# Kernel optimization log

Hardware: AMD Instinct MI355X
Metric: run time of the kernel (lower is better)

## Reference

```python
import jax, jax.numpy as jnp
import numpy as np

D_MODEL = 1024
N_HEADS = 16
D_HEAD = D_MODEL // N_HEADS


def setup_inputs() -> dict:
    key = jax.random.key(0)
    ks = jax.random.split(key, 5)
    scale = 1.0 / np.sqrt(D_MODEL)
    return {
        "x": jax.random.normal(ks[0], (2, 2048, D_MODEL), dtype=jnp.float32),
        "W_q": jax.random.normal(ks[1], (D_MODEL, D_MODEL), dtype=jnp.float32) * scale,
        "W_k": jax.random.normal(ks[2], (D_MODEL, D_MODEL), dtype=jnp.float32) * scale,
        "W_v": jax.random.normal(ks[3], (D_MODEL, D_MODEL), dtype=jnp.float32) * scale,
        "W_o": jax.random.normal(ks[4], (D_MODEL, D_MODEL), dtype=jnp.float32) * scale,
    }


def reference(x, W_q, W_k, W_v, W_o):
    B, S, _ = x.shape
    # nn.Linear computes x @ W.T; weights stored [out, in]
    def proj(W):
        y = jnp.einsum("bsd,ed->bse", x, W)
        return y.reshape(B, S, N_HEADS, D_HEAD).transpose(0, 2, 1, 3)  # [B,H,S,Dh]

    q, k, v = proj(W_q), proj(W_k), proj(W_v)
    scores = jnp.einsum("bhqd,bhkd->bhqk", q, k) / jnp.sqrt(jnp.float32(D_HEAD))
    causal = jnp.triu(jnp.ones((S, S), dtype=bool), k=1)
    scores = jnp.where(causal, -jnp.inf, scores)
    attn = jax.nn.softmax(scores, axis=-1)
    out = jnp.einsum("bhqk,bhkd->bhqd", attn, v)  # [B,H,S,Dh]
    out = out.transpose(0, 2, 1, 3).reshape(B, S, D_MODEL)
    return jnp.einsum("bsd,ed->bse", out, W_o)
```

## Files before the change

kernel.cpp:

```cpp
#include <hip/hip_runtime.h>


#define DMODEL 1024
#define NHEADS 16
#define DHEAD  64
#define SEQ    2048
#define BATCH  2
#define MROWS  (BATCH * SEQ)

typedef __bf16 bf16x8 __attribute__((ext_vector_type(8)));
typedef __bf16 bf16x4 __attribute__((ext_vector_type(4)));
typedef float  f32x4  __attribute__((ext_vector_type(4)));

__device__ __forceinline__ f32x4 mfma16(bf16x8 a, bf16x8 b, f32x4 c) {
    return __builtin_amdgcn_mfma_f32_16x16x32_bf16(a, b, c, 0, 0, 0);
}

__device__ __forceinline__ float max3f(float a, float b, float c) {
    return fmaxf(fmaxf(a, b), c);
}

__device__ __forceinline__ bf16x8 ld8(const float* p) {
    const f32x4 a0 = *(const f32x4*)p;
    const f32x4 a1 = *(const f32x4*)(p + 4);
    bf16x8 v;
    v[0] = (__bf16)a0[0]; v[1] = (__bf16)a0[1];
    v[2] = (__bf16)a0[2]; v[3] = (__bf16)a0[3];
    v[4] = (__bf16)a1[0]; v[5] = (__bf16)a1[1];
    v[6] = (__bf16)a1[2]; v[7] = (__bf16)a1[3];
    return v;
}

__device__ __forceinline__ void gll16(const __bf16* g, __bf16* l) {
    __builtin_amdgcn_global_load_lds(
        (const __attribute__((address_space(1))) void*)g,
        (__attribute__((address_space(3))) void*)l,
        16, 0, 0);
}

__global__ __launch_bounds__(256) void cvt_kernel(const float* __restrict__ x,
                                                  const float* __restrict__ Wq,
                                                  const float* __restrict__ Wk,
                                                  const float* __restrict__ Wv,
                                                  const float* __restrict__ Wo,
                                                  __bf16* __restrict__ xb,
                                                  __bf16* __restrict__ wcat) {
    const int y = blockIdx.y;
    const float* src;
    __bf16* dst;
    int nchunks;
    if (y == 0) { src = x; dst = xb; nchunks = (MROWS * DMODEL) / 8; }
    else {
        src = (y == 1) ? Wq : (y == 2) ? Wk : (y == 3) ? Wv : Wo;
        dst = wcat + (size_t)(y - 1) * DMODEL * DMODEL;
        nchunks = (DMODEL * DMODEL) / 8;
    }
    const int c = blockIdx.x * 256 + threadIdx.x;
    if (c < nchunks) *(bf16x8*)(dst + (size_t)c * 8) = ld8(src + (size_t)c * 8);
}

template <typename TC>
__device__ __forceinline__ void gemm_bb_body(const __bf16* __restrict__ A,
                                             const __bf16* __restrict__ W,
                                             TC* __restrict__ C,
                                             __bf16* __restrict__ VT,
                                             bool vt, int m0, int bn0, int cn0,
                                             float scale) {
    constexpr int K = DMODEL;
    __shared__ __align__(16) __bf16 As[128][32];
    __shared__ __align__(16) __bf16 Bs[128][32];

    const int tid  = threadIdx.x;
    const int lane = tid & 63;
    const int wave = tid >> 6;
    const int quad = lane >> 4;
    const int l16  = lane & 15;
    const int wm   = wave & 1;
    const int wn   = wave >> 1;

    const int srow = lane >> 2;
    const int scol = (lane & 3) * 8;

    const __bf16* a0p = A + (size_t)(m0 + wave * 16 + srow) * K + scol;
    const __bf16* a1p = A + (size_t)(m0 + 64 + wave * 16 + srow) * K + scol;
    const __bf16* b0p = W + (size_t)(bn0 + wave * 16 + srow) * K + scol;
    const __bf16* b1p = W + (size_t)(bn0 + 64 + wave * 16 + srow) * K + scol;

    f32x4 acc[4][4] = {};

    for (int k0 = 0; k0 < K; k0 += 32) {
        __syncthreads();
        gll16(a0p + k0, &As[wave * 16][0]);
        gll16(a1p + k0, &As[64 + wave * 16][0]);
        gll16(b0p + k0, &Bs[wave * 16][0]);
        gll16(b1p + k0, &Bs[64 + wave * 16][0]);
        __syncthreads();

        bf16x8 af[4], bfr[4];
#pragma unroll
        for (int i = 0; i < 4; ++i) {
            af[i]  = *(const bf16x8*)(&As[wm * 64 + i * 16 + l16][quad * 8]);
            bfr[i] = *(const bf16x8*)(&Bs[wn * 64 + i * 16 + l16][quad * 8]);
        }
#pragma unroll
        for (int mi = 0; mi < 4; ++mi)
#pragma unroll
            for (int ni = 0; ni < 4; ++ni)
                acc[mi][ni] = mfma16(af[mi], bfr[ni], acc[mi][ni]);
    }

    if (!vt) {
#pragma unroll
        for (int mi = 0; mi < 4; ++mi)
#pragma unroll
            for (int ni = 0; ni < 4; ++ni)
#pragma unroll
                for (int r = 0; r < 4; ++r) {
                    int row = m0 + wm * 64 + mi * 16 + quad * 4 + r;
                    int col = cn0 + wn * 64 + ni * 16 + l16;
                    C[(size_t)row * DMODEL + col] = (TC)(acc[mi][ni][r] * scale);
                }
    } else {
#pragma unroll
        for (int mi = 0; mi < 4; ++mi)
#pragma unroll
            for (int ni = 0; ni < 4; ++ni) {
                const int m  = m0 + wm * 64 + mi * 16 + quad * 4;
                const int hd = cn0 + wn * 64 + ni * 16 + l16;
                bf16x4 v4;
#pragma unroll
                for (int r = 0; r < 4; ++r) v4[r] = (__bf16)acc[mi][ni][r];
                *(bf16x4*)(VT + (size_t)hd * MROWS + m) = v4;
            }
    }
}

#define QSCALE 0.1803368801111204f

__global__ __launch_bounds__(256) void qkv_kernel(const __bf16* __restrict__ X,
                                                  const __bf16* __restrict__ wcat,
                                                  __bf16* __restrict__ Q,
                                                  __bf16* __restrict__ K,
                                                  __bf16* __restrict__ VT) {
    const int bn0 = blockIdx.x * 128;
    const int z   = bn0 >> 10;
    const int cn0 = bn0 - (z << 10);
    __bf16* Y = (z == 0) ? Q : K;
    const float scale = (z == 0) ? QSCALE : 1.0f;
    gemm_bb_body<__bf16>(X, wcat, Y, VT, z == 2,
                         blockIdx.y * 128, bn0, cn0, scale);
}

__global__ __launch_bounds__(256) void out_gemm_kernel(const __bf16* __restrict__ A,
                                                       const __bf16* __restrict__ W,
                                                       float* __restrict__ C) {
    gemm_bb_body<float>(A, W, C, nullptr, false,
                        blockIdx.y * 128, blockIdx.x * 128, blockIdx.x * 128, 1.0f);
}

__global__ __launch_bounds__(256) void attn_kernel(const __bf16* __restrict__ Q,
                                                   const __bf16* __restrict__ Kg,
                                                   const __bf16* __restrict__ VTg,
                                                   __bf16* __restrict__ O) {
    const int bh  = blockIdx.x;
    const int y   = blockIdx.y;
    const int ya  = y >> 3, yr = y & 7;
    const int qt2 = (ya == 0) ? (31 - yr)
                  : (ya == 1) ? (16 + yr)
                  : (ya == 2) ? (15 - yr)
                  :             yr;
    const int b = bh >> 4, h = bh & 15;
    const size_t base = (size_t)b * SEQ * DMODEL + (size_t)h * DHEAD;

    const int tid  = threadIdx.x;
    const int lane = tid & 63;
    const int wave = tid >> 6;
    const int quad = lane >> 4;
    const int l16  = lane & 15;

    __shared__ __align__(16) __bf16 Ks[64][64];
    __shared__ __align__(16) __bf16 Vs[64][64];
    __shared__ __align__(16) __bf16 Ps[4][2][16][40];

    const int sr = lane >> 3;
    const int sc = ((lane & 7) ^ sr) * 8;

    const int qrow = qt2 * 64 + wave * 16 + l16;

    const bf16x8 qf0 = *(const bf16x8*)(Q + base + (size_t)qrow * DMODEL + quad * 8);
    const bf16x8 qf1 = *(const bf16x8*)(Q + base + (size_t)qrow * DMODEL + 32 + quad * 8);

    const __bf16* kp = Kg + base + (size_t)(wave * 16 + sr) * DMODEL + sc;
    const __bf16* vp = VTg + (size_t)(h * 64 + wave * 16 + sr) * MROWS
                           + (size_t)b * SEQ + sc;

    bf16x8 ones;
#pragma unroll
    for (int i = 0; i < 8; ++i) ones[i] = (__bf16)1.0f;

    f32x4 oacc[4] = {};
    f32x4 lacc = {};
    float m_i = -1e30f;

    const int ntiles = qt2 + 1;
    const int gsw = (l16 & 7);

    for (int kt = 0; kt < ntiles; ++kt) {
        const int k0 = kt * 64;
        __syncthreads();
        {
            const __bf16* kpt = kp + (size_t)k0 * DMODEL;
            const __bf16* vpt = vp + k0;
            gll16(kpt, &Ks[wave * 16][0]);
            gll16(kpt + (size_t)8 * DMODEL, &Ks[wave * 16 + 8][0]);
            gll16(vpt, &Vs[wave * 16][0]);
            gll16(vpt + (size_t)8 * MROWS, &Vs[wave * 16 + 8][0]);
        }
        __syncthreads();

        const bool diag = (kt == ntiles - 1);

        f32x4 s[4];
#pragma unroll
        for (int g = 0; g < 4; ++g) {
            const bf16x8 kfa = *(const bf16x8*)(&Ks[g * 16 + l16][(quad ^ gsw) * 8]);
            const bf16x8 kfb = *(const bf16x8*)(&Ks[g * 16 + l16][((quad + 4) ^ gsw) * 8]);
            f32x4 t = {};
            t = mfma16(kfa, qf0, t);
            t = mfma16(kfb, qf1, t);
            s[g] = t;
        }

        float mx;
        bool ok[4][4];
        if (!diag) {
            const float t0 = max3f(s[0][0], s[0][1], s[0][2]);
            const float t1 = max3f(s[0][3], s[1][0], s[1][1]);
            const float t2 = max3f(s[1][2], s[1][3], s[2][0]);
            const float t3 = max3f(s[2][1], s[2][2], s[2][3]);
            const float t4 = max3f(s[3][0], s[3][1], s[3][2]);
            mx = max3f(max3f(t0, t1, t2), fmaxf(t3, t4), s[3][3]);
        } else {
            float v[4][4];
#pragma unroll
            for (int g = 0; g < 4; ++g)
#pragma unroll
                for (int r = 0; r < 4; ++r) {
                    const int kk = k0 + g * 16 + quad * 4 + r;
                    ok[g][r] = (kk <= qrow);
                    v[g][r] = ok[g][r] ? s[g][r] : -1e30f;
                }
            const float t0 = max3f(v[0][0], v[0][1], v[0][2]);
            const float t1 = max3f(v[0][3], v[1][0], v[1][1]);
            const float t2 = max3f(v[1][2], v[1][3], v[2][0]);
            const float t3 = max3f(v[2][1], v[2][2], v[2][3]);
            const float t4 = max3f(v[3][0], v[3][1], v[3][2]);
            mx = max3f(max3f(t0, t1, t2), fmaxf(t3, t4), v[3][3]);
        }
        mx = fmaxf(mx, __shfl_xor(mx, 16));
        mx = fmaxf(mx, __shfl_xor(mx, 32));

        const bool defer = __all(mx - m_i <= 8.0f);
        float mnew;
        if (defer) {
            mnew = m_i;
        } else {
            mnew = fmaxf(m_i, mx);
            const float alpha = exp2f(m_i - mnew);
            m_i = mnew;
#pragma unroll
            for (int f = 0; f < 4; ++f) oacc[f] *= alpha;
            lacc *= alpha;
        }

        bf16x4 w4[4];
        if (!diag) {
#pragma unroll
            for (int g = 0; g < 4; ++g)
#pragma unroll
                for (int r = 0; r < 4; ++r)
                    w4[g][r] = (__bf16)exp2f(s[g][r] - mnew);
        } else {
#pragma unroll
            for (int g = 0; g < 4; ++g)
#pragma unroll
                for (int r = 0; r < 4; ++r)
                    w4[g][r] = (__bf16)(ok[g][r] ? exp2f(s[g][r] - mnew) : 0.f);
        }

#pragma unroll
        for (int g = 0; g < 4; ++g)
            *(bf16x4*)(&Ps[wave][g >> 1][l16][(g & 1) * 16 + quad * 4]) = w4[g];

        const bf16x8 pf0 = *(const bf16x8*)(&Ps[wave][0][l16][quad * 8]);
        const bf16x8 pf1 = *(const bf16x8*)(&Ps[wave][1][l16][quad * 8]);
        lacc = mfma16(ones, pf0, lacc);
        lacc = mfma16(ones, pf1, lacc);
#pragma unroll
        for (int f = 0; f < 4; ++f) {
            const bf16x8 vfa = *(const bf16x8*)(&Vs[f * 16 + l16][(quad ^ gsw) * 8]);
            const bf16x8 vfb = *(const bf16x8*)(&Vs[f * 16 + l16][((quad + 4) ^ gsw) * 8]);
            f32x4 t = oacc[f];
            t = mfma16(vfa, pf0, t);
            t = mfma16(vfb, pf1, t);
            oacc[f] = t;
        }
    }

    const float l_i = lacc[0];
    const float inv = (l_i > 0.f) ? (1.f / l_i) : 0.f;
#pragma unroll
    for (int f = 0; f < 4; ++f) {
        bf16x4 o;
#pragma unroll
        for (int r = 0; r < 4; ++r) o[r] = (__bf16)(oacc[f][r] * inv);
        *(bf16x4*)(O + base + (size_t)qrow * DMODEL + f * 16 + quad * 4) = o;
    }
}

extern "C" void kernel_launch(void* const* d_in, const int* in_sizes, int n_in,
                              void* d_out, int out_size, void* d_ws, size_t ws_size,
                              hipStream_t stream) {
    const float* x  = (const float*)d_in[0];
    const float* Wq = (const float*)d_in[1];
    const float* Wk = (const float*)d_in[2];
    const float* Wv = (const float*)d_in[3];
    const float* Wo = (const float*)d_in[4];
    float* out = (float*)d_out;

    const size_t tm = (size_t)MROWS * DMODEL;
    const size_t tw = (size_t)DMODEL * DMODEL;
    __bf16* Q    = (__bf16*)d_ws;
    __bf16* K    = Q + tm;
    __bf16* VT   = K + tm;
    __bf16* xb   = VT + tm;
    __bf16* wcat = xb + tm;

    dim3 gc(2048, 5);
    cvt_kernel<<<gc, 256, 0, stream>>>(x, Wq, Wk, Wv, Wo, xb, wcat);

    dim3 g1(3072 / 128, MROWS / 128);
    qkv_kernel<<<g1, 256, 0, stream>>>(xb, wcat, Q, K, VT);

    dim3 g2(BATCH * NHEADS, SEQ / 64);
    attn_kernel<<<g2, 256, 0, stream>>>(Q, K, VT, Q);

    dim3 g3(DMODEL / 128, MROWS / 128);
    out_gemm_kernel<<<g3, 256, 0, stream>>>(Q, wcat + 3 * tw, out);
}
```

Measured before the change: 186.6 us.

## Deepen GEMM K-tile to 64 with XOR-swizzled LDS and smaller output tiles

The shared GEMM body now stages 64-wide K slices instead of 32. LDS columns are XOR-swizzled to avoid bank conflicts on fragment reads, and the kernel is templated on M-tile size. This halves the number of barrier pairs per GEMM. The output projection uses 64-row tiles to launch more blocks, and the conversion kernel is flattened into a 1D grid with no idle blocks. Doubling the LDS tile size may lower occupancy.

Measured after the change: 183.7 us. About the same (-1.5%).

```diff
diff --git a/kernel.cpp b/kernel.cpp
--- a/kernel.cpp
+++ b/kernel.cpp
@@ -45,21 +45,20 @@
                                                   const float* __restrict__ Wo,
                                                   __bf16* __restrict__ xb,
                                                   __bf16* __restrict__ wcat) {
-    const int y = blockIdx.y;
-    const float* src;
-    __bf16* dst;
-    int nchunks;
-    if (y == 0) { src = x; dst = xb; nchunks = (MROWS * DMODEL) / 8; }
-    else {
-        src = (y == 1) ? Wq : (y == 2) ? Wk : (y == 3) ? Wv : Wo;
-        dst = wcat + (size_t)(y - 1) * DMODEL * DMODEL;
-        nchunks = (DMODEL * DMODEL) / 8;
-    }
     const int c = blockIdx.x * 256 + threadIdx.x;
-    if (c < nchunks) *(bf16x8*)(dst + (size_t)c * 8) = ld8(src + (size_t)c * 8);
-}
-
-template <typename TC>
+    if (c < 524288) {
+        *(bf16x8*)(xb + (size_t)c * 8) = ld8(x + (size_t)c * 8);
+    } else {
+        const int i = c - 524288;
+        const int w = i >> 17;
+        const int j = i & 131071;
+        const float* src = (w == 0) ? Wq : (w == 1) ? Wk : (w == 2) ? Wv : Wo;
+        *(bf16x8*)(wcat + (size_t)w * DMODEL * DMODEL + (size_t)j * 8) =
+            ld8(src + (size_t)j * 8);
+    }
+}
+
+template <typename TC, int MI>
 __device__ __forceinline__ void gemm_bb_body(const __bf16* __restrict__ A,
                                              const __bf16* __restrict__ W,
                                              TC* __restrict__ C,
@@ -67,8 +66,9 @@
                                              bool vt, int m0, int bn0, int cn0,
                                              float scale) {
     constexpr int K = DMODEL;
-    __shared__ __align__(16) __bf16 As[128][32];
-    __shared__ __align__(16) __bf16 Bs[128][32];
+    constexpr int TM = MI * 32;
+    __shared__ __align__(16) __bf16 As[TM][64];
+    __shared__ __align__(16) __bf16 Bs[128][64];
 
     const int tid  = threadIdx.x;
     const int lane = tid & 63;
@@ -78,54 +78,63 @@
     const int wm   = wave & 1;
     const int wn   = wave >> 1;
 
-    const int srow = lane >> 2;
-    const int scol = (lane & 3) * 8;
-
-    const __bf16* a0p = A + (size_t)(m0 + wave * 16 + srow) * K + scol;
-    const __bf16* a1p = A + (size_t)(m0 + 64 + wave * 16 + srow) * K + scol;
-    const __bf16* b0p = W + (size_t)(bn0 + wave * 16 + srow) * K + scol;
-    const __bf16* b1p = W + (size_t)(bn0 + 64 + wave * 16 + srow) * K + scol;
-
-    f32x4 acc[4][4] = {};
-
-    for (int k0 = 0; k0 < K; k0 += 32) {
+    const int sr8 = lane >> 3;
+    const int scs = ((lane & 7) ^ sr8) * 8;
+
+    const int g8 = l16 & 7;
+
+    f32x4 acc[MI][4] = {};
+
+    for (int k0 = 0; k0 < K; k0 += 64) {
         __syncthreads();
-        gll16(a0p + k0, &As[wave * 16][0]);
-        gll16(a1p + k0, &As[64 + wave * 16][0]);
-        gll16(b0p + k0, &Bs[wave * 16][0]);
-        gll16(b1p + k0, &Bs[64 + wave * 16][0]);
+#pragma unroll
+        for (int j = 0; j < MI; ++j) {
+            const int row = wave * (MI * 8) + j * 8;
+            gll16(A + (size_t)(m0 + row + sr8) * K + k0 + scs, &As[row][0]);
+        }
+#pragma unroll
+        for (int j = 0; j < 4; ++j) {
+            const int row = wave * 32 + j * 8;
+            gll16(W + (size_t)(bn0 + row + sr8) * K + k0 + scs, &Bs[row][0]);
+        }
         __syncthreads();
 
-        bf16x8 af[4], bfr[4];
-#pragma unroll
-        for (int i = 0; i < 4; ++i) {
-            af[i]  = *(const bf16x8*)(&As[wm * 64 + i * 16 + l16][quad * 8]);
-            bfr[i] = *(const bf16x8*)(&Bs[wn * 64 + i * 16 + l16][quad * 8]);
-        }
-#pragma unroll
-        for (int mi = 0; mi < 4; ++mi)
+#pragma unroll
+        for (int h = 0; h < 2; ++h) {
+            bf16x8 af[MI], bfr[4];
+#pragma unroll
+            for (int i = 0; i < MI; ++i)
+                af[i] = *(const bf16x8*)(
+                    &As[wm * (MI * 16) + i * 16 + l16][((h * 4 + quad) ^ g8) * 8]);
+#pragma unroll
+            for (int j = 0; j < 4; ++j)
+                bfr[j] = *(const bf16x8*)(
+                    &Bs[wn * 64 + j * 16 + l16][((h * 4 + quad) ^ g8) * 8]);
+#pragma unroll
+            for (int mi = 0; mi < MI; ++mi)
+#pragma unroll
+                for (int ni = 0; ni < 4; ++ni)
+                    acc[mi][ni] = mfma16(af[mi], bfr[ni], acc[mi][ni]);
+        }
+    }
+
+    if (!vt) {
+#pragma unroll
+        for (int mi = 0; mi < MI; ++mi)
 #pragma unroll
             for (int ni = 0; ni < 4; ++ni)
-                acc[mi][ni] = mfma16(af[mi], bfr[ni], acc[mi][ni]);
-    }
-
-    if (!vt) {
-#pragma unroll
-        for (int mi = 0; mi < 4; ++mi)
-#pragma unroll
-            for (int ni = 0; ni < 4; ++ni)
 #pragma unroll
                 for (int r = 0; r < 4; ++r) {
-                    int row = m0 + wm * 64 + mi * 16 + quad * 4 + r;
+                    int row = m0 + wm * (MI * 16) + mi * 16 + quad * 4 + r;
                     int col = cn0 + wn * 64 + ni * 16 + l16;
                     C[(size_t)row * DMODEL + col] = (TC)(acc[mi][ni][r] * scale);
                 }
     } else {
 #pragma unroll
-        for (int mi = 0; mi < 4; ++mi)
+        for (int mi = 0; mi < MI; ++mi)
 #pragma unroll
             for (int ni = 0; ni < 4; ++ni) {
-                const int m  = m0 + wm * 64 + mi * 16 + quad * 4;
+                const int m  = m0 + wm * (MI * 16) + mi * 16 + quad * 4;
                 const int hd = cn0 + wn * 64 + ni * 16 + l16;
                 bf16x4 v4;
 #pragma unroll
@@ -147,15 +156,16 @@
     const int cn0 = bn0 - (z << 10);
     __bf16* Y = (z == 0) ? Q : K;
     const float scale = (z == 0) ? QSCALE : 1.0f;
-    gemm_bb_body<__bf16>(X, wcat, Y, VT, z == 2,
-                         blockIdx.y * 128, bn0, cn0, scale);
+    gemm_bb_body<__bf16, 4>(X, wcat, Y, VT, z == 2,
+                            blockIdx.y * 128, bn0, cn0, scale);
 }
 
 __global__ __launch_bounds__(256) void out_gemm_kernel(const __bf16* __restrict__ A,
                                                        const __bf16* __restrict__ W,
                                                        float* __restrict__ C) {
-    gemm_bb_body<float>(A, W, C, nullptr, false,
-                        blockIdx.y * 128, blockIdx.x * 128, blockIdx.x * 128, 1.0f);
+    gemm_bb_body<float, 2>(A, W, C, nullptr, false,
+                           blockIdx.y * 64, blockIdx.x * 128, blockIdx.x * 128,
+                           1.0f);
 }
 
 __global__ __launch_bounds__(256) void attn_kernel(const __bf16* __restrict__ Q,
@@ -336,8 +346,7 @@
     __bf16* xb   = VT + tm;
     __bf16* wcat = xb + tm;
 
-    dim3 gc(2048, 5);
-    cvt_kernel<<<gc, 256, 0, stream>>>(x, Wq, Wk, Wv, Wo, xb, wcat);
+    cvt_kernel<<<4096, 256, 0, stream>>>(x, Wq, Wk, Wv, Wo, xb, wcat);
 
     dim3 g1(3072 / 128, MROWS / 128);
     qkv_kernel<<<g1, 256, 0, stream>>>(xb, wcat, Q, K, VT);
@@ -345,6 +354,6 @@
     dim3 g2(BATCH * NHEADS, SEQ / 64);
     attn_kernel<<<g2, 256, 0, stream>>>(Q, K, VT, Q);
 
-    dim3 g3(DMODEL / 128, MROWS / 128);
+    dim3 g3(DMODEL / 128, MROWS / 64);
     out_gemm_kernel<<<g3, 256, 0, stream>>>(Q, wcat + 3 * tw, out);
 }
```
